# Optimization experiments

Hardware: AMD Instinct MI355X
Metric: run time of the kernel (lower is better)

## Reference

```python
import jax, jax.numpy as jnp
import numpy as np


def setup_inputs() -> dict:
    key = jax.random.key(0)
    k1, k2 = jax.random.split(key)
    B, Ld, Lq, D = 32, 2048, 512, 256
    doc = jax.random.normal(k1, (B, Ld, D), dtype=jnp.float32)
    query = jax.random.normal(k2, (B, Lq, D), dtype=jnp.float32)
    doc_mask = jnp.ones((B, Ld), dtype=jnp.float32)
    q_mask = jnp.ones((B, Lq), dtype=jnp.float32)
    return {"doc": doc, "query": query, "doc_mask": doc_mask, "q_mask": q_mask}


def reference(doc, query, doc_mask, q_mask):
    # match_score: [B, Lq, Ld] = tanh(query @ doc^T)
    match_score = jnp.tanh(jnp.einsum('bqd,btd->bqt', query, doc))
    # sum over query positions -> [B, Ld]; softmax over doc positions
    query_to_doc_att = jax.nn.softmax(jnp.sum(match_score, axis=1), axis=-1)
    # sum over doc positions -> [B, Lq]; softmax over query positions
    doc_to_query_att = jax.nn.softmax(jnp.sum(match_score, axis=-1), axis=-1)
    # mask and renormalize
    alpha = query_to_doc_att * doc_mask
    alpha = alpha / jnp.sum(alpha, axis=1, keepdims=True)
    beta = doc_to_query_att * q_mask
    beta = beta / jnp.sum(beta, axis=1, keepdims=True)
    # weighted pooling: doc^T @ alpha -> [B, D]; query^T @ beta -> [B, D]
    doc_vector = jnp.einsum('btd,bt->bd', doc, alpha)
    que_vector = jnp.einsum('bqd,bq->bd', query, beta)
    return jnp.concatenate([doc_vector, que_vector], axis=1)  # [B, 2D]
```

## Files before the change

### kernel.cpp

```cpp
#include <hip/hip_runtime.h>
#include <hip/hip_bf16.h>
#include <cstdint>

#define BB 32
#define LD 2048
#define LQ 512
#define DD 256
#define BM 128
#define BN 128
#define BK 64

typedef _Float16 half8 __attribute__((ext_vector_type(8)));
typedef _Float16 half4 __attribute__((ext_vector_type(4)));
typedef float float4v __attribute__((ext_vector_type(4)));

__device__ __forceinline__ float tanh_fast(float x) {
    float t = __builtin_amdgcn_exp2f(x * 2.885390081777927f);
    float r = __builtin_amdgcn_rcpf(t + 1.0f);
    return fmaf(-2.0f, r, 1.0f);
}

__device__ __forceinline__ void load_lds16(const void* g, void* s) {
    __builtin_amdgcn_global_load_lds((const __attribute__((address_space(1))) void*)g,
                                     (__attribute__((address_space(3))) void*)s, 16, 0, 0);
}

#define DOCN8 (BB * LD * DD / 8)
#define QRYN8 (BB * LQ * DD / 8)

__global__ __launch_bounds__(256) void kconv(const float* __restrict__ doc,
                                             const float* __restrict__ qry,
                                             _Float16* __restrict__ dh,
                                             _Float16* __restrict__ qh) {
    int i = blockIdx.x * 256 + threadIdx.x;
    const float* src;
    _Float16* dst;
    int idx;
    if (i < DOCN8) { src = doc; dst = dh; idx = i; }
    else           { src = qry; dst = qh; idx = i - DOCN8; }
    const float4v* s = (const float4v*)src + (size_t)idx * 2;
    float4v a = s[0], c = s[1];
    half8 h = {(_Float16)a[0], (_Float16)a[1], (_Float16)a[2], (_Float16)a[3],
               (_Float16)c[0], (_Float16)c[1], (_Float16)c[2], (_Float16)c[3]};
    *((half8*)dst + idx) = h;
}

template <bool F16SRC>
__global__ __launch_bounds__(256, 4) void k1(const void* __restrict__ qsrc,
                                             const void* __restrict__ dsrc,
                                             float* __restrict__ pa,
                                             float* __restrict__ pb) {
    __shared__ _Float16 sQ[BM * BK];
    __shared__ _Float16 sD[BN * BK];
    __shared__ float srow[BM][2];
    __shared__ float scol[BN][2];
    const int bq = blockIdx.x, bt = blockIdx.y, b = blockIdx.z;
    const int tid = threadIdx.x;
    const int lane = tid & 63;
    const int wave = tid >> 6;
    const int r16 = lane & 15;
    const int q4 = lane >> 4;
    const int mb = (wave >> 1) * 64, nb = (wave & 1) * 64;

    float4v acc[4][4];
    float4v zero = {0.f, 0.f, 0.f, 0.f};
#pragma unroll
    for (int m = 0; m < 4; m++)
#pragma unroll
        for (int n = 0; n < 4; n++) acc[m][n] = zero;

    const int lrow = lane >> 3;
    const int lcol = ((lane & 7) ^ lrow) * 8;

    for (int kk = 0; kk < DD; kk += BK) {
        __syncthreads();
        if constexpr (F16SRC) {
            const _Float16* Qh = (const _Float16*)qsrc + ((size_t)b * LQ + bq * BM) * DD;
            const _Float16* Dh = (const _Float16*)dsrc + ((size_t)b * LD + bt * BN) * DD;
#pragma unroll
            for (int j = 0; j < 4; j++) {
                int c = wave * 4 + j;
                int row = 8 * c + lrow;
                load_lds16(Qh + (size_t)row * DD + kk + lcol, &sQ[c * 512]);
                load_lds16(Dh + (size_t)row * DD + kk + lcol, &sD[c * 512]);
            }
        } else {
            const float* Qf = (const float*)qsrc + ((size_t)b * LQ + bq * BM) * DD;
            const float* Df = (const float*)dsrc + ((size_t)b * LD + bt * BN) * DD;
#pragma unroll
            for (int i = 0; i < 8; i++) {
                int f = tid + 256 * i;
                int row = f >> 4, c = f & 15;
                int c2 = c >> 1, hlf = c & 1;
                int p = c2 ^ (row & 7);
                float4v v = *(const float4v*)(Qf + (size_t)row * DD + kk + 4 * c);
                half4 h = {(_Float16)v[0], (_Float16)v[1], (_Float16)v[2], (_Float16)v[3]};
                *(half4*)(&sQ[row * BK + p * 8 + hlf * 4]) = h;
                float4v w = *(const float4v*)(Df + (size_t)row * DD + kk + 4 * c);
                half4 h2 = {(_Float16)w[0], (_Float16)w[1], (_Float16)w[2], (_Float16)w[3]};
                *(half4*)(&sD[row * BK + p * 8 + hlf * 4]) = h2;
            }
        }
        __syncthreads();

#pragma unroll
        for (int kk2 = 0; kk2 < 2; kk2++) {
            const int sw = ((4 * kk2 + q4) ^ (r16 & 7)) * 8;
            half8 af[4], bf[4];
#pragma unroll
            for (int m = 0; m < 4; m++) af[m] = *(const half8*)(&sQ[(mb + 16 * m + r16) * BK + sw]);
#pragma unroll
            for (int n = 0; n < 4; n++) bf[n] = *(const half8*)(&sD[(nb + 16 * n + r16) * BK + sw]);
#pragma unroll
            for (int m = 0; m < 4; m++)
#pragma unroll
                for (int n = 0; n < 4; n++)
                    acc[m][n] = __builtin_amdgcn_mfma_f32_16x16x32_f16(af[m], bf[n], acc[m][n], 0, 0, 0);
        }
    }

    float rsum[4][4];
    float csum[4];
#pragma unroll
    for (int m = 0; m < 4; m++)
#pragma unroll
        for (int r = 0; r < 4; r++) rsum[m][r] = 0.f;
#pragma unroll
    for (int n = 0; n < 4; n++) csum[n] = 0.f;

#pragma unroll
    for (int m = 0; m < 4; m++)
#pragma unroll
        for (int n = 0; n < 4; n++) {
            float t0 = tanh_fast(acc[m][n][0]);
            float t1 = tanh_fast(acc[m][n][1]);
            float t2 = tanh_fast(acc[m][n][2]);
            float t3 = tanh_fast(acc[m][n][3]);
            csum[n] += t0 + t1 + t2 + t3;
            rsum[m][0] += t0;
            rsum[m][1] += t1;
            rsum[m][2] += t2;
            rsum[m][3] += t3;
        }

#pragma unroll
    for (int m = 0; m < 4; m++) {
#pragma unroll
        for (int r = 0; r < 4; r++) {
            float v = rsum[m][r];
            v += __shfl_xor(v, 1);
            v += __shfl_xor(v, 2);
            v += __shfl_xor(v, 4);
            v += __shfl_xor(v, 8);
            rsum[m][r] = v;
        }
        if (r16 < 4) {
            float v = (r16 == 0) ? rsum[m][0] : (r16 == 1) ? rsum[m][1] : (r16 == 2) ? rsum[m][2] : rsum[m][3];
            srow[mb + 16 * m + 4 * q4 + r16][wave & 1] = v;
        }
    }
#pragma unroll
    for (int n = 0; n < 4; n++) {
        float v = csum[n];
        v += __shfl_xor(v, 16);
        v += __shfl_xor(v, 32);
        if (lane < 16) scol[nb + 16 * n + lane][wave >> 1] = v;
    }
    __syncthreads();
    if (tid < 128) {
        float v = srow[tid][0] + srow[tid][1];
        pb[((size_t)bt * BB + b) * LQ + bq * BM + tid] = v;
        float u = scol[tid][0] + scol[tid][1];
        pa[((size_t)bq * BB + b) * LD + bt * BN + tid] = u;
    }
}

template <bool F16SRC>
__global__ __launch_bounds__(256) void k23(const float* __restrict__ pa, const float* __restrict__ pb,
                                           const float* __restrict__ dmask, const float* __restrict__ qmask,
                                           const float* __restrict__ docf, const float* __restrict__ qryf,
                                           const _Float16* __restrict__ dh, const _Float16* __restrict__ qh,
                                           float* __restrict__ out) {
    __shared__ float sl[2048];
    __shared__ float sred[32][64];
    __shared__ float sm[4], ss[4];
    const int blk = blockIdx.x, tid = threadIdx.x, lane = tid & 63, wave = tid >> 6;
    const bool isdoc = blk < 128;
    const int k = isdoc ? blk : blk - 128;
    const int b = k >> 2, dc = k & 3;
    const int n = isdoc ? LD : LQ;
    const float* mk = isdoc ? dmask + (size_t)b * LD : qmask + (size_t)b * LQ;

    if (isdoc) {
        for (int i = tid; i < n; i += 256) {
            float s = 0.f;
#pragma unroll
            for (int j = 0; j < 4; j++) s += pa[((size_t)j * BB + b) * LD + i];
            sl[i] = s;
        }
    } else {
        for (int i = tid; i < n; i += 256) {
            float s = 0.f;
#pragma unroll
            for (int j = 0; j < 16; j++) s += pb[((size_t)j * BB + b) * LQ + i];
            sl[i] = s;
        }
    }
    __syncthreads();
    float mx = -3.0e38f;
    for (int i = tid; i < n; i += 256) mx = fmaxf(mx, sl[i]);
#pragma unroll
    for (int s = 1; s < 64; s <<= 1) mx = fmaxf(mx, __shfl_xor(mx, s));
    if (lane == 0) sm[wave] = mx;
    __syncthreads();
    mx = fmaxf(fmaxf(sm[0], sm[1]), fmaxf(sm[2], sm[3]));
    const float L2E = 1.4426950408889634f;
    float sum = 0.f;
    for (int i = tid; i < n; i += 256) {
        float e = __builtin_amdgcn_exp2f((sl[i] - mx) * L2E) * mk[i];
        sl[i] = e;
        sum += e;
    }
#pragma unroll
    for (int s = 1; s < 64; s <<= 1) sum += __shfl_xor(sum, s);
    if (lane == 0) ss[wave] = sum;
    __syncthreads();
    sum = ss[0] + ss[1] + ss[2] + ss[3];
    const float inv = 1.0f / sum;

    const int c8 = tid & 7, pg = tid >> 3;
    const int per = n >> 5;
    float acc[8];
#pragma unroll
    for (int j = 0; j < 8; j++) acc[j] = 0.f;
    const int dof = dc * 64 + c8 * 8;
    if constexpr (F16SRC) {
        const _Float16* src = (isdoc ? dh + (size_t)b * LD * DD : qh + (size_t)b * LQ * DD) + dof;
        for (int r = 0; r < per; r++) {
            int t = pg * per + r;
            float wt = sl[t];
            half8 x = *(const half8*)(src + (size_t)t * DD);
#pragma unroll
            for (int j = 0; j < 8; j++) acc[j] += wt * (float)x[j];
        }
    } else {
        const float* src = (isdoc ? docf + (size_t)b * LD * DD : qryf + (size_t)b * LQ * DD) + dof;
        for (int r = 0; r < per; r++) {
            int t = pg * per + r;
            float wt = sl[t];
            const float4v* p = (const float4v*)(src + (size_t)t * DD);
            float4v x0 = p[0], x1 = p[1];
#pragma unroll
            for (int j = 0; j < 4; j++) { acc[j] += wt * x0[j]; acc[4 + j] += wt * x1[j]; }
        }
    }
#pragma unroll
    for (int j = 0; j < 8; j++) sred[pg][c8 * 8 + j] = acc[j];
    __syncthreads();
    if (tid < 64) {
        float s = 0.f;
#pragma unroll
        for (int g = 0; g < 32; g++) s += sred[g][tid];
        out[(size_t)b * 2 * DD + (isdoc ? 0 : DD) + dc * 64 + tid] = s * inv;
    }
}

extern "C" void kernel_launch(void* const* d_in, const int* in_sizes, int n_in,
                              void* d_out, int out_size, void* d_ws, size_t ws_size,
                              hipStream_t stream) {
    (void)in_sizes; (void)n_in; (void)out_size;
    const float* doc = (const float*)d_in[0];
    const float* qry = (const float*)d_in[1];
    const float* dmask = (const float*)d_in[2];
    const float* qmask = (const float*)d_in[3];
    float* out = (float*)d_out;

    float* pa = (float*)d_ws;
    float* pb = pa + 4 * BB * LD;
    _Float16* dh = (_Float16*)(pb + 16 * BB * LQ);
    _Float16* qh = dh + (size_t)BB * LD * DD;
    size_t needed = (size_t)(4 * BB * LD + 16 * BB * LQ) * 4 +
                    ((size_t)BB * LD * DD + (size_t)BB * LQ * DD) * 2;
    bool useF16 = ws_size >= needed;

    if (useF16) {
        kconv<<<(DOCN8 + QRYN8) / 256, 256, 0, stream>>>(doc, qry, dh, qh);
        k1<true><<<dim3(LQ / BM, LD / BN, BB), 256, 0, stream>>>(qh, dh, pa, pb);
        k23<true><<<256, 256, 0, stream>>>(pa, pb, dmask, qmask, doc, qry, dh, qh, out);
    } else {
        k1<false><<<dim3(LQ / BM, LD / BN, BB), 256, 0, stream>>>(qry, doc, pa, pb);
        k23<false><<<256, 256, 0, stream>>>(pa, pb, dmask, qmask, doc, qry, dh, qh, out);
    }
}
```

Measured before the change: 157.0 us.

## Double-buffer LDS tiles with async global_load_lds and waitcnt-based pipelining

The f16-source GEMM path now uses two LDS buffers per operand. The next K-slice is issued via global_load_lds while the current slice feeds the MFMAs, and completion is tracked with explicit s_waitcnt vmcnt plus raw barriers instead of __syncthreads. The goal is to hide global-to-LDS latency behind matrix math. In exchange, LDS use doubles, which may cut occupancy below the requested 4 blocks per CU. Correctness also depends on the hand-coded waitcnt immediates matching the number of outstanding loads.

```diff
diff --git a/kernel.cpp b/kernel.cpp
--- a/kernel.cpp
+++ b/kernel.cpp
@@ -24,6 +24,9 @@
     __builtin_amdgcn_global_load_lds((const __attribute__((address_space(1))) void*)g,
                                      (__attribute__((address_space(3))) void*)s, 16, 0, 0);
 }
+
+#define WAITCNT_VM8 0xF78
+#define WAITCNT_VM0 0xF70
 
 #define DOCN8 (BB * LD * DD / 8)
 #define QRYN8 (BB * LQ * DD / 8)
@@ -50,8 +53,8 @@
                                              const void* __restrict__ dsrc,
                                              float* __restrict__ pa,
                                              float* __restrict__ pb) {
-    __shared__ _Float16 sQ[BM * BK];
-    __shared__ _Float16 sD[BN * BK];
+    __shared__ _Float16 sQ[2][BM * BK];
+    __shared__ _Float16 sD[2][BN * BK];
     __shared__ float srow[BM][2];
     __shared__ float scol[BN][2];
     const int bq = blockIdx.x, bt = blockIdx.y, b = blockIdx.z;
@@ -72,19 +75,52 @@
     const int lrow = lane >> 3;
     const int lcol = ((lane & 7) ^ lrow) * 8;
 
-    for (int kk = 0; kk < DD; kk += BK) {
-        __syncthreads();
-        if constexpr (F16SRC) {
-            const _Float16* Qh = (const _Float16*)qsrc + ((size_t)b * LQ + bq * BM) * DD;
-            const _Float16* Dh = (const _Float16*)dsrc + ((size_t)b * LD + bt * BN) * DD;
-#pragma unroll
-            for (int j = 0; j < 4; j++) {
-                int c = wave * 4 + j;
-                int row = 8 * c + lrow;
-                load_lds16(Qh + (size_t)row * DD + kk + lcol, &sQ[c * 512]);
-                load_lds16(Dh + (size_t)row * DD + kk + lcol, &sD[c * 512]);
+    const _Float16* Qh = (const _Float16*)qsrc + ((size_t)b * LQ + bq * BM) * DD;
+    const _Float16* Dh = (const _Float16*)dsrc + ((size_t)b * LD + bt * BN) * DD;
+
+    auto stage = [&](int kk, int buf) {
+#pragma unroll
+        for (int j = 0; j < 4; j++) {
+            int c = wave * 4 + j;
+            int row = 8 * c + lrow;
+            load_lds16(Qh + (size_t)row * DD + kk + lcol, &sQ[buf][c * 512]);
+            load_lds16(Dh + (size_t)row * DD + kk + lcol, &sD[buf][c * 512]);
+        }
+    };
+
+    if constexpr (F16SRC) {
+        stage(0, 0);
+        stage(BK, 1);
+#pragma unroll
+        for (int kk4 = 0; kk4 < 4; kk4++) {
+            const int bsel = kk4 & 1;
+            if (kk4 < 3) __builtin_amdgcn_s_waitcnt(WAITCNT_VM8);
+            else         __builtin_amdgcn_s_waitcnt(WAITCNT_VM0);
+            asm volatile("" ::: "memory");
+            __builtin_amdgcn_s_barrier();
+            asm volatile("" ::: "memory");
+#pragma unroll
+            for (int kk2 = 0; kk2 < 2; kk2++) {
+                const int sw = ((4 * kk2 + q4) ^ (r16 & 7)) * 8;
+                half8 af[4], bf[4];
+#pragma unroll
+                for (int m = 0; m < 4; m++) af[m] = *(const half8*)(&sQ[bsel][(mb + 16 * m + r16) * BK + sw]);
+#pragma unroll
+                for (int n = 0; n < 4; n++) bf[n] = *(const half8*)(&sD[bsel][(nb + 16 * n + r16) * BK + sw]);
+#pragma unroll
+                for (int m = 0; m < 4; m++)
+#pragma unroll
+                    for (int n = 0; n < 4; n++)
+                        acc[m][n] = __builtin_amdgcn_mfma_f32_16x16x32_f16(af[m], bf[n], acc[m][n], 0, 0, 0);
             }
-        } else {
+            asm volatile("" ::: "memory");
+            __builtin_amdgcn_s_barrier();
+            asm volatile("" ::: "memory");
+            if (kk4 < 2) stage((kk4 + 2) * BK, bsel);
+        }
+    } else {
+        for (int kk = 0; kk < DD; kk += BK) {
+            __syncthreads();
             const float* Qf = (const float*)qsrc + ((size_t)b * LQ + bq * BM) * DD;
             const float* Df = (const float*)dsrc + ((size_t)b * LD + bt * BN) * DD;
 #pragma unroll
@@ -95,27 +131,26 @@
                 int p = c2 ^ (row & 7);
                 float4v v = *(const float4v*)(Qf + (size_t)row * DD + kk + 4 * c);
                 half4 h = {(_Float16)v[0], (_Float16)v[1], (_Float16)v[2], (_Float16)v[3]};
-                *(half4*)(&sQ[row * BK + p * 8 + hlf * 4]) = h;
+                *(half4*)(&sQ[0][row * BK + p * 8 + hlf * 4]) = h;
                 float4v w = *(const float4v*)(Df + (size_t)row * DD + kk + 4 * c);
                 half4 h2 = {(_Float16)w[0], (_Float16)w[1], (_Float16)w[2], (_Float16)w[3]};
-                *(half4*)(&sD[row * BK + p * 8 + hlf * 4]) = h2;
+                *(half4*)(&sD[0][row * BK + p * 8 + hlf * 4]) = h2;
             }
-        }
-        __syncthreads();
-
-#pragma unroll
-        for (int kk2 = 0; kk2 < 2; kk2++) {
-            const int sw = ((4 * kk2 + q4) ^ (r16 & 7)) * 8;
-            half8 af[4], bf[4];
-#pragma unroll
-            for (int m = 0; m < 4; m++) af[m] = *(const half8*)(&sQ[(mb + 16 * m + r16) * BK + sw]);
-#pragma unroll
-            for (int n = 0; n < 4; n++) bf[n] = *(const half8*)(&sD[(nb + 16 * n + r16) * BK + sw]);
-#pragma unroll
-            for (int m = 0; m < 4; m++)
-#pragma unroll
-                for (int n = 0; n < 4; n++)
-                    acc[m][n] = __builtin_amdgcn_mfma_f32_16x16x32_f16(af[m], bf[n], acc[m][n], 0, 0, 0);
+            __syncthreads();
+#pragma unroll
+            for (int kk2 = 0; kk2 < 2; kk2++) {
+                const int sw = ((4 * kk2 + q4) ^ (r16 & 7)) * 8;
+                half8 af[4], bf[4];
+#pragma unroll
+                for (int m = 0; m < 4; m++) af[m] = *(const half8*)(&sQ[0][(mb + 16 * m + r16) * BK + sw]);
+#pragma unroll
+                for (int n = 0; n < 4; n++) bf[n] = *(const half8*)(&sD[0][(nb + 16 * n + r16) * BK + sw]);
+#pragma unroll
+                for (int m = 0; m < 4; m++)
+#pragma unroll
+                    for (int n = 0; n < 4; n++)
+                        acc[m][n] = __builtin_amdgcn_mfma_f32_16x16x32_f16(af[m], bf[n], acc[m][n], 0, 0, 0);
+            }
         }
     }
 
```

Result: slower. 162.5 us (+3.5%).
